# Performance work log

Measured on AMD Instinct MI355X. Metric: run time of the kernel, lower is better.

The kernel has to match this reference:

```python
import jax, jax.numpy as jnp
import numpy as np

N = 50000   # nodes
E = 800000  # edges (avg degree 16)
D = 96      # input feature dim
U = 96      # units (== D, so no dense_i projection)


def _glorot(key, fan_in, fan_out):
    limit = np.sqrt(6.0 / (fan_in + fan_out)).astype(np.float32)
    return jax.random.uniform(key, (fan_in, fan_out), jnp.float32, -limit, limit)


def setup_inputs() -> dict:
    key = jax.random.key(0)
    ks = jax.random.split(key, 8)
    X = jax.random.normal(ks[0], (N, D), jnp.float32)
    row = jax.random.randint(ks[1], (E,), 0, N, jnp.int32)   # destination nodes
    col = jax.random.randint(ks[2], (E,), 0, N, jnp.int32)   # source nodes
    a_vals = jax.random.uniform(ks[3], (E,), jnp.float32)    # adjacency values
    return {
        "X": X,
        "a_vals": a_vals,
        "Wn": _glorot(ks[4], D, U), "bn": jnp.zeros((U,), jnp.float32),
        "Wgi": _glorot(ks[5], D, U), "bgi": jnp.zeros((U,), jnp.float32),
        "Wgn": _glorot(ks[6], U, U), "bgn": jnp.zeros((U,), jnp.float32),
        "row": row, "col": col,
    }


def reference(X, a_vals, Wn, bn, Wgi, bgi, Wgn, bgn, row, col):
    # new_X = dense_n(X); new_X = A @ new_X  (SpMM via gather + segment_sum)
    newX = X @ Wn + bn                       # [N, U]
    msgs = a_vals[:, None] * newX[col]       # [E, U]
    agg = jax.ops.segment_sum(msgs, row, num_segments=N)  # [N, U]
    # gate = sigmoid(dense_gate_i(X) + dense_gate_n(agg))
    gate = jax.nn.sigmoid(X @ Wgi + bgi + agg @ Wgn + bgn)
    # units == inp_dim -> no dense_i; gated residual combine
    return agg * gate + X * (1.0 - gate)
```

## Files before the change

kernel.cpp:

```cpp
#include <hip/hip_runtime.h>
#include <math.h>


#define DU 96
#define DU4 24
#define NSUB 64
#define NGRP 8
#define HMAX 6656

typedef unsigned int uint;
typedef unsigned short ushort;
typedef __attribute__((ext_vector_type(8))) short short8;
typedef __attribute__((ext_vector_type(4))) float f32x4;

__device__ inline uint bf16r(float x) {
  uint u = __float_as_uint(x);
  return (u + 0x7FFFu + ((u >> 16) & 1u)) >> 16;
}

__global__ __launch_bounds__(256) void k_fuse1(
    const float* __restrict__ X, const float* __restrict__ Wn,
    const float* __restrict__ bn, const float* __restrict__ Wgi,
    const float* __restrict__ Wgn, const int* __restrict__ row,
    ushort* __restrict__ Xb, ushort* __restrict__ newXb,
    ushort* __restrict__ WTgi, ushort* __restrict__ WTgn,
    ushort* __restrict__ pc, int N, int E, int ntile) {
  __shared__ __align__(16) char smem[31744];
  ushort* WL = (ushort*)smem;
  typedef ushort XsRow[104];
  XsRow* Xs = (XsRow*)(smem + 18432);
  const int tid = threadIdx.x;
  const int lane = tid & 63, w = tid >> 6;
  const int m = lane & 15, q = lane >> 4;

  if ((int)blockIdx.x < ntile) {
    if (blockIdx.x == 0) {
      for (int i = tid; i < DU * DU; i += 256) {
        int n = i / DU, k = i % DU;
        WTgi[i] = (ushort)bf16r(Wgi[k * DU + n]);
      }
    } else if (blockIdx.x == 1) {
      for (int i = tid; i < DU * DU; i += 256) {
        int n = i / DU, k = i % DU;
        WTgn[i] = (ushort)bf16r(Wgn[k * DU + n]);
      }
    }
    for (int idx = tid; idx < 9216; idx += 256) {
      int j = idx & 7, ln = (idx >> 3) & 63, tk = idx >> 9;
      int ks = tk / 6, t = tk % 6;
      int k = ks * 32 + (ln >> 4) * 8 + j;
      int n = t * 16 + (ln & 15);
      WL[idx] = (ushort)bf16r(Wn[k * DU + n]);
    }
    const int row0 = blockIdx.x * 64;
    for (int i = tid; i < 64 * 48; i += 256) {
      int r = i / 48, cu = i % 48;
      int gr = row0 + r;
      uint packed = 0;
      if (gr < N) {
        float2 v = ((const float2*)X)[(size_t)gr * 48 + cu];
        packed = bf16r(v.x) | (bf16r(v.y) << 16);
        ((uint*)Xb)[(size_t)gr * 48 + cu] = packed;
      }
      *(uint*)&Xs[r][cu * 2] = packed;
    }
    __syncthreads();

    f32x4 acc[6];
#pragma unroll
    for (int t = 0; t < 6; ++t) acc[t] = (f32x4){0.f, 0.f, 0.f, 0.f};
#pragma unroll
    for (int ks = 0; ks < 3; ++ks) {
      short8 af = *(const short8*)&Xs[w * 16 + m][ks * 32 + q * 8];
#pragma unroll
      for (int t = 0; t < 6; ++t) {
        short8 bf = *(const short8*)&WL[((ks * 6 + t) * 64 + lane) * 8];
        acc[t] = __builtin_amdgcn_mfma_f32_16x16x32_bf16(af, bf, acc[t], 0, 0, 0);
      }
    }
    __syncthreads();
#pragma unroll
    for (int t = 0; t < 6; ++t) {
      int c = t * 16 + m;
      float bb = bn[c];
#pragma unroll
      for (int i = 0; i < 4; ++i)
        Xs[w * 16 + q * 4 + i][c] = (ushort)bf16r(acc[t][i] + bb);
    }
    __syncthreads();
    for (int i = tid; i < 64 * 48; i += 256) {
      int r = i / 48, cu = i % 48;
      int gr = row0 + r;
      if (gr < N) ((uint*)newXb)[(size_t)gr * 48 + cu] = *(uint*)&Xs[r][cu * 2];
    }
  } else {
    int* hist = (int*)smem;
    const int hb = (int)blockIdx.x - ntile;
    const int g = (int)(blockIdx.x & 7);
    const int sub = hb >> 3;
    const int d0 = (int)((long long)N * g >> 3);
    const int d1 = (int)((long long)N * (g + 1) >> 3);
    const int hs = d1 - d0;
    for (int j = tid; j < hs; j += 256) hist[j] = 0;
    __syncthreads();
    const int e0 = (int)(((long long)E * sub) >> 6);
    const int e1 = (int)(((long long)E * (sub + 1)) >> 6);
    int i = e0 + tid;
    for (; i + 1792 < e1; i += 2048) {
      int a0 = row[i], a1 = row[i + 256], a2 = row[i + 512], a3 = row[i + 768];
      int a4 = row[i + 1024], a5 = row[i + 1280], a6 = row[i + 1536], a7 = row[i + 1792];
      if (a0 >= d0 && a0 < d1) atomicAdd(&hist[a0 - d0], 1);
      if (a1 >= d0 && a1 < d1) atomicAdd(&hist[a1 - d0], 1);
      if (a2 >= d0 && a2 < d1) atomicAdd(&hist[a2 - d0], 1);
      if (a3 >= d0 && a3 < d1) atomicAdd(&hist[a3 - d0], 1);
      if (a4 >= d0 && a4 < d1) atomicAdd(&hist[a4 - d0], 1);
      if (a5 >= d0 && a5 < d1) atomicAdd(&hist[a5 - d0], 1);
      if (a6 >= d0 && a6 < d1) atomicAdd(&hist[a6 - d0], 1);
      if (a7 >= d0 && a7 < d1) atomicAdd(&hist[a7 - d0], 1);
    }
    for (; i < e1; i += 256) {
      int d = row[i];
      if (d >= d0 && d < d1) atomicAdd(&hist[d - d0], 1);
    }
    __syncthreads();
    for (int j = tid; j < hs; j += 256) pc[(size_t)sub * N + d0 + j] = (ushort)hist[j];
  }
}

__global__ __launch_bounds__(256) void k_colsum(const ushort* __restrict__ pc,
                                                ushort* __restrict__ psub, int N) {
  int d2 = (blockIdx.x * 256 + threadIdx.x) * 2;
  if (d2 >= N) return;
  int runLo = 0, runHi = 0;
#pragma unroll 8
  for (int s = 0; s < NSUB; ++s) {
    uint v = *(const uint*)(pc + (size_t)s * N + d2);
    *(uint*)(psub + (size_t)s * N + d2) = (uint)runLo | ((uint)runHi << 16);
    runLo += (int)(v & 0xFFFFu);
    runHi += (int)(v >> 16);
  }
}

__global__ __launch_bounds__(1024) void k_scan(const ushort* __restrict__ pc,
                                               const ushort* __restrict__ psub,
                                               int* __restrict__ off, int N) {
  __shared__ int ws[16];
  __shared__ int carry_s;
  const ushort* pcL = pc + (size_t)(NSUB - 1) * N;
  const ushort* psL = psub + (size_t)(NSUB - 1) * N;
  const int tid = threadIdx.x;
  const int lane = tid & 63, wid = tid >> 6;
  if (tid == 0) carry_s = 0;
  __syncthreads();
  const int PT = 8;
  const int CH = 1024 * PT;
  for (int base = 0; base < N; base += CH) {
    int idx = base + tid * PT;
    int tot[PT];
    int s = 0;
    if (idx < N) {
      uint4 a = *(const uint4*)(pcL + idx);
      uint4 b = *(const uint4*)(psL + idx);
      tot[0] = (int)(a.x & 0xFFFFu) + (int)(b.x & 0xFFFFu);
      tot[1] = (int)(a.x >> 16) + (int)(b.x >> 16);
      tot[2] = (int)(a.y & 0xFFFFu) + (int)(b.y & 0xFFFFu);
      tot[3] = (int)(a.y >> 16) + (int)(b.y >> 16);
      tot[4] = (int)(a.z & 0xFFFFu) + (int)(b.z & 0xFFFFu);
      tot[5] = (int)(a.z >> 16) + (int)(b.z >> 16);
      tot[6] = (int)(a.w & 0xFFFFu) + (int)(b.w & 0xFFFFu);
      tot[7] = (int)(a.w >> 16) + (int)(b.w >> 16);
#pragma unroll
      for (int j = 0; j < PT; ++j) s += tot[j];
    } else {
#pragma unroll
      for (int j = 0; j < PT; ++j) tot[j] = 0;
    }
    int incl = s;
#pragma unroll
    for (int d = 1; d < 64; d <<= 1) {
      int t = __shfl_up(incl, d, 64);
      if (lane >= d) incl += t;
    }
    if (lane == 63) ws[wid] = incl;
    __syncthreads();
    int carry = carry_s;
    int wexcl = 0;
#pragma unroll
    for (int k = 0; k < 16; ++k)
      if (k < wid) wexcl += ws[k];
    int running = carry + wexcl + (incl - s);
    if (idx < N) {
      int4 o1, o2;
      o1.x = running; running += tot[0];
      o1.y = running; running += tot[1];
      o1.z = running; running += tot[2];
      o1.w = running; running += tot[3];
      o2.x = running; running += tot[4];
      o2.y = running; running += tot[5];
      o2.z = running; running += tot[6];
      o2.w = running; running += tot[7];
      ((int4*)(off + idx))[0] = o1;
      ((int4*)(off + idx))[1] = o2;
    }
    __syncthreads();
    if (tid == 0) {
      int t16 = 0;
#pragma unroll
      for (int k = 0; k < 16; ++k) t16 += ws[k];
      carry_s += t16;
    }
    __syncthreads();
  }
  if (tid == 0) off[N] = carry_s;
}

__global__ __launch_bounds__(256) void k_scatter(const int* __restrict__ row,
                                                 const int* __restrict__ col,
                                                 const float* __restrict__ a_vals,
                                                 const int* __restrict__ off,
                                                 const ushort* __restrict__ psub,
                                                 int2* __restrict__ ec,
                                                 int N, int E) {
  __shared__ int cur[HMAX];
  const int g = (int)(blockIdx.x & 7);
  const int sub = (int)(blockIdx.x >> 3);
  const int d0 = (int)((long long)N * g >> 3);
  const int d1 = (int)((long long)N * (g + 1) >> 3);
  const int hs = d1 - d0;
  for (int j = threadIdx.x; j < hs; j += 256)
    cur[j] = off[d0 + j] + (int)psub[(size_t)sub * N + d0 + j];
  __syncthreads();
  const int e0 = (int)(((long long)E * sub) >> 6);
  const int e1 = (int)(((long long)E * (sub + 1)) >> 6);
  int i = e0 + (int)threadIdx.x;
  for (; i + 1792 < e1; i += 2048) {
    int a0 = row[i], a1 = row[i + 256], a2 = row[i + 512], a3 = row[i + 768];
    int a4 = row[i + 1024], a5 = row[i + 1280], a6 = row[i + 1536], a7 = row[i + 1792];
    if (a0 >= d0 && a0 < d1) {
      int s = atomicAdd(&cur[a0 - d0], 1);
      ec[s] = make_int2(col[i], __float_as_int(a_vals[i]));
    }
    if (a1 >= d0 && a1 < d1) {
      int s = atomicAdd(&cur[a1 - d0], 1);
      ec[s] = make_int2(col[i + 256], __float_as_int(a_vals[i + 256]));
    }
    if (a2 >= d0 && a2 < d1) {
      int s = atomicAdd(&cur[a2 - d0], 1);
      ec[s] = make_int2(col[i + 512], __float_as_int(a_vals[i + 512]));
    }
    if (a3 >= d0 && a3 < d1) {
      int s = atomicAdd(&cur[a3 - d0], 1);
      ec[s] = make_int2(col[i + 768], __float_as_int(a_vals[i + 768]));
    }
    if (a4 >= d0 && a4 < d1) {
      int s = atomicAdd(&cur[a4 - d0], 1);
      ec[s] = make_int2(col[i + 1024], __float_as_int(a_vals[i + 1024]));
    }
    if (a5 >= d0 && a5 < d1) {
      int s = atomicAdd(&cur[a5 - d0], 1);
      ec[s] = make_int2(col[i + 1280], __float_as_int(a_vals[i + 1280]));
    }
    if (a6 >= d0 && a6 < d1) {
      int s = atomicAdd(&cur[a6 - d0], 1);
      ec[s] = make_int2(col[i + 1536], __float_as_int(a_vals[i + 1536]));
    }
    if (a7 >= d0 && a7 < d1) {
      int s = atomicAdd(&cur[a7 - d0], 1);
      ec[s] = make_int2(col[i + 1792], __float_as_int(a_vals[i + 1792]));
    }
  }
  for (; i < e1; i += 256) {
    int d = row[i];
    if (d >= d0 && d < d1) {
      int s = atomicAdd(&cur[d - d0], 1);
      ec[s] = make_int2(col[i], __float_as_int(a_vals[i]));
    }
  }
}

__global__ __launch_bounds__(256) void k_agg(const ushort* __restrict__ newXb,
                                             const int* __restrict__ off,
                                             const int2* __restrict__ ec,
                                             ushort* __restrict__ aggb, int N) {
  const int g = (int)(blockIdx.x & 7);
  const int b2 = (int)(blockIdx.x >> 3);
  const int d0 = (int)((long long)N * g >> 3);
  const int ntask = ((int)((long long)N * (g + 1) >> 3) - d0) * 12;
  int i = b2 * 256 + threadIdx.x;
  if (i >= ntask) return;
  int r = d0 + i / 12;
  int c = i % 12;
  int o0 = off[r];
  int e1 = off[r + 1] - o0;
  const int2* ep = ec + o0;
  float accA[8], accB[8];
#pragma unroll
  for (int k = 0; k < 8; ++k) { accA[k] = 0.f; accB[k] = 0.f; }
  int e = 0;
#define GCN_FMA8(ACC, V, A)                                      \
  ACC[0] = fmaf(A, __uint_as_float(V.x << 16), ACC[0]);          \
  ACC[1] = fmaf(A, __uint_as_float(V.x & 0xFFFF0000u), ACC[1]);  \
  ACC[2] = fmaf(A, __uint_as_float(V.y << 16), ACC[2]);          \
  ACC[3] = fmaf(A, __uint_as_float(V.y & 0xFFFF0000u), ACC[3]);  \
  ACC[4] = fmaf(A, __uint_as_float(V.z << 16), ACC[4]);          \
  ACC[5] = fmaf(A, __uint_as_float(V.z & 0xFFFF0000u), ACC[5]);  \
  ACC[6] = fmaf(A, __uint_as_float(V.w << 16), ACC[6]);          \
  ACC[7] = fmaf(A, __uint_as_float(V.w & 0xFFFF0000u), ACC[7])
  for (; e + 8 <= e1; e += 8) {
    int2 p0 = ep[e + 0];
    int2 p1 = ep[e + 1];
    int2 p2 = ep[e + 2];
    int2 p3 = ep[e + 3];
    int2 p4 = ep[e + 4];
    int2 p5 = ep[e + 5];
    int2 p6 = ep[e + 6];
    int2 p7 = ep[e + 7];
    uint4 v0 = *(const uint4*)(newXb + (size_t)p0.x * DU + c * 8);
    uint4 v1 = *(const uint4*)(newXb + (size_t)p1.x * DU + c * 8);
    uint4 v2 = *(const uint4*)(newXb + (size_t)p2.x * DU + c * 8);
    uint4 v3 = *(const uint4*)(newXb + (size_t)p3.x * DU + c * 8);
    uint4 v4 = *(const uint4*)(newXb + (size_t)p4.x * DU + c * 8);
    uint4 v5 = *(const uint4*)(newXb + (size_t)p5.x * DU + c * 8);
    uint4 v6 = *(const uint4*)(newXb + (size_t)p6.x * DU + c * 8);
    uint4 v7 = *(const uint4*)(newXb + (size_t)p7.x * DU + c * 8);
    float a0 = __int_as_float(p0.y), a1 = __int_as_float(p1.y);
    float a2 = __int_as_float(p2.y), a3 = __int_as_float(p3.y);
    float a4 = __int_as_float(p4.y), a5 = __int_as_float(p5.y);
    float a6 = __int_as_float(p6.y), a7 = __int_as_float(p7.y);
    GCN_FMA8(accA, v0, a0);
    GCN_FMA8(accB, v1, a1);
    GCN_FMA8(accA, v2, a2);
    GCN_FMA8(accB, v3, a3);
    GCN_FMA8(accA, v4, a4);
    GCN_FMA8(accB, v5, a5);
    GCN_FMA8(accA, v6, a6);
    GCN_FMA8(accB, v7, a7);
  }
  for (; e + 4 <= e1; e += 4) {
    int2 p0 = ep[e + 0];
    int2 p1 = ep[e + 1];
    int2 p2 = ep[e + 2];
    int2 p3 = ep[e + 3];
    uint4 v0 = *(const uint4*)(newXb + (size_t)p0.x * DU + c * 8);
    uint4 v1 = *(const uint4*)(newXb + (size_t)p1.x * DU + c * 8);
    uint4 v2 = *(const uint4*)(newXb + (size_t)p2.x * DU + c * 8);
    uint4 v3 = *(const uint4*)(newXb + (size_t)p3.x * DU + c * 8);
    float a0 = __int_as_float(p0.y), a1 = __int_as_float(p1.y);
    float a2 = __int_as_float(p2.y), a3 = __int_as_float(p3.y);
    GCN_FMA8(accA, v0, a0);
    GCN_FMA8(accB, v1, a1);
    GCN_FMA8(accA, v2, a2);
    GCN_FMA8(accB, v3, a3);
  }
  for (; e < e1; ++e) {
    int2 p = ep[e];
    uint4 v = *(const uint4*)(newXb + (size_t)p.x * DU + c * 8);
    float a = __int_as_float(p.y);
    GCN_FMA8(accA, v, a);
  }
#undef GCN_FMA8
#pragma unroll
  for (int k = 0; k < 8; ++k) accA[k] += accB[k];
  uint4 o;
  o.x = bf16r(accA[0]) | (bf16r(accA[1]) << 16);
  o.y = bf16r(accA[2]) | (bf16r(accA[3]) << 16);
  o.z = bf16r(accA[4]) | (bf16r(accA[5]) << 16);
  o.w = bf16r(accA[6]) | (bf16r(accA[7]) << 16);
  *(uint4*)(aggb + (size_t)r * DU + c * 8) = o;
}

__global__ __launch_bounds__(256) void k_gateM(const ushort* __restrict__ Xb,
                                               const ushort* __restrict__ aggb,
                                               const ushort* __restrict__ WTgi,
                                               const ushort* __restrict__ WTgn,
                                               const float* __restrict__ bgi,
                                               const float* __restrict__ bgn,
                                               const float* __restrict__ X,
                                               float* __restrict__ Out, int N) {
  __shared__ float Gs[64][100];
  const int tid = threadIdx.x;
  const int lane = tid & 63, w = tid >> 6;
  const int m = lane & 15, q = lane >> 4;
  const int row0 = blockIdx.x * 64;
  int ar = row0 + w * 16 + m;
  if (ar > N - 1) ar = N - 1;

  f32x4 acc[6];
#pragma unroll
  for (int t = 0; t < 6; ++t) acc[t] = (f32x4){0.f, 0.f, 0.f, 0.f};

#pragma unroll
  for (int ks = 0; ks < 3; ++ks) {
    short8 af = *(const short8*)(Xb + (size_t)ar * DU + ks * 32 + q * 8);
#pragma unroll
    for (int t = 0; t < 6; ++t) {
      short8 bf = *(const short8*)(WTgi + (size_t)(t * 16 + m) * DU + ks * 32 + q * 8);
      acc[t] = __builtin_amdgcn_mfma_f32_16x16x32_bf16(af, bf, acc[t], 0, 0, 0);
    }
  }
#pragma unroll
  for (int ks = 0; ks < 3; ++ks) {
    short8 af = *(const short8*)(aggb + (size_t)ar * DU + ks * 32 + q * 8);
#pragma unroll
    for (int t = 0; t < 6; ++t) {
      short8 bf = *(const short8*)(WTgn + (size_t)(t * 16 + m) * DU + ks * 32 + q * 8);
      acc[t] = __builtin_amdgcn_mfma_f32_16x16x32_bf16(af, bf, acc[t], 0, 0, 0);
    }
  }

#pragma unroll
  for (int t = 0; t < 6; ++t) {
    int c = t * 16 + m;
    float bb = bgi[c] + bgn[c];
#pragma unroll
    for (int i = 0; i < 4; ++i) {
      float z = acc[t][i] + bb;
      Gs[w * 16 + q * 4 + i][c] = 1.f / (1.f + __expf(-z));
    }
  }
  __syncthreads();

  for (int j = tid; j < 64 * DU4; j += 256) {
    int r = j / DU4, c = j % DU4;
    int gr = row0 + r;
    if (gr < N) {
      float4 xv = ((const float4*)X)[(size_t)gr * DU4 + c];
      uint2 av = ((const uint2*)aggb)[(size_t)gr * DU4 + c];
      float a0 = __uint_as_float(av.x << 16);
      float a1 = __uint_as_float(av.x & 0xFFFF0000u);
      float a2 = __uint_as_float(av.y << 16);
      float a3 = __uint_as_float(av.y & 0xFFFF0000u);
      const float* gp = &Gs[r][c * 4];
      float4 o;
      o.x = xv.x + gp[0] * (a0 - xv.x);
      o.y = xv.y + gp[1] * (a1 - xv.y);
      o.z = xv.z + gp[2] * (a2 - xv.z);
      o.w = xv.w + gp[3] * (a3 - xv.w);
      ((float4*)Out)[(size_t)gr * DU4 + c] = o;
    }
  }
}

extern "C" void kernel_launch(void* const* d_in, const int* in_sizes, int n_in,
                              void* d_out, int out_size, void* d_ws, size_t ws_size,
                              hipStream_t stream) {
  const float* X      = (const float*)d_in[0];
  const float* a_vals = (const float*)d_in[1];
  const float* Wn     = (const float*)d_in[2];
  const float* bn     = (const float*)d_in[3];
  const float* Wgi    = (const float*)d_in[4];
  const float* bgi    = (const float*)d_in[5];
  const float* Wgn    = (const float*)d_in[6];
  const float* bgn    = (const float*)d_in[7];
  const int*   row    = (const int*)d_in[8];
  const int*   col    = (const int*)d_in[9];
  float* out = (float*)d_out;

  const int N = in_sizes[0] / DU;
  const int E = in_sizes[1];
  const int ntile = (N + 63) / 64;
  const int G1 = ntile + NSUB * NGRP;

  int2*   ec    = (int2*)d_ws;
  ushort* Xb    = (ushort*)(ec + (size_t)E);
  ushort* newXb = Xb + (size_t)N * DU;
  ushort* aggb  = newXb + (size_t)N * DU;
  ushort* WTgi  = aggb + (size_t)N * DU;
  ushort* WTgn  = WTgi + DU * DU;
  int*    off   = (int*)(WTgn + DU * DU);
  ushort* pc    = (ushort*)(off + ((N + 4) & ~3));
  ushort* psub  = pc + (size_t)NSUB * N;

  const int aggBPG = (int)(((long long)N * 12 / 8 + 255) / 256);

  k_fuse1  <<<G1, 256, 0, stream>>>(X, Wn, bn, Wgi, Wgn, row,
                                    Xb, newXb, WTgi, WTgn, pc, N, E, ntile);
  k_colsum <<<(N / 2 + 255) / 256, 256, 0, stream>>>(pc, psub, N);
  k_scan   <<<1, 1024, 0, stream>>>(pc, psub, off, N);
  k_scatter<<<NSUB * NGRP, 256, 0, stream>>>(row, col, a_vals, off, psub, ec, N, E);
  k_agg    <<<aggBPG * NGRP, 256, 0, stream>>>(newXb, off, ec, aggb, N);
  k_gateM  <<<ntile, 256, 0, stream>>>(Xb, aggb, WTgi, WTgn, bgi, bgn, X, out, N);
}
```

Measured before the change: 196.6 us.

## Fuse aggregation into gate kernel and merge colsum/scan into per-group prep

The SpMM aggregation is fused into the gate kernel, so per-tile aggregates stay in shared memory as fp32 and are never written to or read back from a bf16 buffer. The column-sum and single-block scan are replaced by one kernel with 8 blocks that scans each destination group independently, using fixed padded per-group capacities in the edge buffer so no global scan is needed. NSUB is halved to 32 to shorten the histogram and colsum work. In exchange, the fused kernel runs only ntile blocks, each doing a serial gather before its MFMA work, which lowers parallelism in the gather phase. The padded capacity assumes no group exceeds E/8 plus 16384 edges, which holds for uniform random rows but could overflow on skewed graphs.

```diff
diff --git a/kernel.cpp b/kernel.cpp
--- a/kernel.cpp
+++ b/kernel.cpp
@@ -4,9 +4,10 @@
 
 #define DU 96
 #define DU4 24
-#define NSUB 64
+#define NSUB 32
 #define NGRP 8
 #define HMAX 6656
+#define CAPG_PAD 16384
 
 typedef unsigned int uint;
 typedef unsigned short ushort;
@@ -103,8 +104,8 @@
     const int hs = d1 - d0;
     for (int j = tid; j < hs; j += 256) hist[j] = 0;
     __syncthreads();
-    const int e0 = (int)(((long long)E * sub) >> 6);
-    const int e1 = (int)(((long long)E * (sub + 1)) >> 6);
+    const int e0 = (int)(((long long)E * sub) / NSUB);
+    const int e1 = (int)(((long long)E * (sub + 1)) / NSUB);
     int i = e0 + tid;
     for (; i + 1792 < e1; i += 2048) {
       int a0 = row[i], a1 = row[i + 256], a2 = row[i + 512], a3 = row[i + 768];
@@ -127,91 +128,63 @@
   }
 }
 
-__global__ __launch_bounds__(256) void k_colsum(const ushort* __restrict__ pc,
-                                                ushort* __restrict__ psub, int N) {
-  int d2 = (blockIdx.x * 256 + threadIdx.x) * 2;
-  if (d2 >= N) return;
-  int runLo = 0, runHi = 0;
-#pragma unroll 8
-  for (int s = 0; s < NSUB; ++s) {
-    uint v = *(const uint*)(pc + (size_t)s * N + d2);
-    *(uint*)(psub + (size_t)s * N + d2) = (uint)runLo | ((uint)runHi << 16);
-    runLo += (int)(v & 0xFFFFu);
-    runHi += (int)(v >> 16);
-  }
-}
-
-__global__ __launch_bounds__(1024) void k_scan(const ushort* __restrict__ pc,
-                                               const ushort* __restrict__ psub,
-                                               int* __restrict__ off, int N) {
+__global__ __launch_bounds__(1024) void k_prep(const ushort* __restrict__ pc,
+                                               ushort* __restrict__ psub,
+                                               ushort* __restrict__ deg,
+                                               int* __restrict__ off,
+                                               int N, int E) {
+  __shared__ ushort degs[HMAX];
   __shared__ int ws[16];
-  __shared__ int carry_s;
-  const ushort* pcL = pc + (size_t)(NSUB - 1) * N;
-  const ushort* psL = psub + (size_t)(NSUB - 1) * N;
+  const int g = blockIdx.x;
   const int tid = threadIdx.x;
   const int lane = tid & 63, wid = tid >> 6;
-  if (tid == 0) carry_s = 0;
+  const int d0 = (int)((long long)N * g >> 3);
+  const int d1 = (int)((long long)N * (g + 1) >> 3);
+  const int hs = d1 - d0;
+  for (int j2 = tid * 2; j2 < hs; j2 += 2048) {
+    int d2 = d0 + j2;
+    int runLo = 0, runHi = 0;
+#pragma unroll 8
+    for (int s = 0; s < NSUB; ++s) {
+      uint v = *(const uint*)(pc + (size_t)s * N + d2);
+      *(uint*)(psub + (size_t)s * N + d2) = (uint)runLo | ((uint)runHi << 16);
+      runLo += (int)(v & 0xFFFFu);
+      runHi += (int)(v >> 16);
+    }
+    uint dpair = (uint)runLo | ((uint)runHi << 16);
+    *(uint*)&degs[j2] = dpair;
+    *(uint*)(deg + d2) = dpair;
+  }
   __syncthreads();
   const int PT = 8;
-  const int CH = 1024 * PT;
-  for (int base = 0; base < N; base += CH) {
-    int idx = base + tid * PT;
-    int tot[PT];
-    int s = 0;
-    if (idx < N) {
-      uint4 a = *(const uint4*)(pcL + idx);
-      uint4 b = *(const uint4*)(psL + idx);
-      tot[0] = (int)(a.x & 0xFFFFu) + (int)(b.x & 0xFFFFu);
-      tot[1] = (int)(a.x >> 16) + (int)(b.x >> 16);
-      tot[2] = (int)(a.y & 0xFFFFu) + (int)(b.y & 0xFFFFu);
-      tot[3] = (int)(a.y >> 16) + (int)(b.y >> 16);
-      tot[4] = (int)(a.z & 0xFFFFu) + (int)(b.z & 0xFFFFu);
-      tot[5] = (int)(a.z >> 16) + (int)(b.z >> 16);
-      tot[6] = (int)(a.w & 0xFFFFu) + (int)(b.w & 0xFFFFu);
-      tot[7] = (int)(a.w >> 16) + (int)(b.w >> 16);
-#pragma unroll
-      for (int j = 0; j < PT; ++j) s += tot[j];
-    } else {
-#pragma unroll
-      for (int j = 0; j < PT; ++j) tot[j] = 0;
-    }
-    int incl = s;
-#pragma unroll
-    for (int d = 1; d < 64; d <<= 1) {
-      int t = __shfl_up(incl, d, 64);
-      if (lane >= d) incl += t;
-    }
-    if (lane == 63) ws[wid] = incl;
-    __syncthreads();
-    int carry = carry_s;
-    int wexcl = 0;
-#pragma unroll
-    for (int k = 0; k < 16; ++k)
-      if (k < wid) wexcl += ws[k];
-    int running = carry + wexcl + (incl - s);
-    if (idx < N) {
-      int4 o1, o2;
-      o1.x = running; running += tot[0];
-      o1.y = running; running += tot[1];
-      o1.z = running; running += tot[2];
-      o1.w = running; running += tot[3];
-      o2.x = running; running += tot[4];
-      o2.y = running; running += tot[5];
-      o2.z = running; running += tot[6];
-      o2.w = running; running += tot[7];
-      ((int4*)(off + idx))[0] = o1;
-      ((int4*)(off + idx))[1] = o2;
-    }
-    __syncthreads();
-    if (tid == 0) {
-      int t16 = 0;
-#pragma unroll
-      for (int k = 0; k < 16; ++k) t16 += ws[k];
-      carry_s += t16;
-    }
-    __syncthreads();
-  }
-  if (tid == 0) off[N] = carry_s;
+  const int j0 = tid * PT;
+  int v[PT];
+  int s = 0;
+#pragma unroll
+  for (int k = 0; k < PT; ++k) {
+    int j = j0 + k;
+    v[k] = (j < hs) ? (int)degs[j] : 0;
+    s += v[k];
+  }
+  int incl = s;
+#pragma unroll
+  for (int dlt = 1; dlt < 64; dlt <<= 1) {
+    int t = __shfl_up(incl, dlt, 64);
+    if (lane >= dlt) incl += t;
+  }
+  if (lane == 63) ws[wid] = incl;
+  __syncthreads();
+  int wexcl = 0;
+#pragma unroll
+  for (int k = 0; k < 16; ++k)
+    if (k < wid) wexcl += ws[k];
+  const int capg = (E >> 3) + CAPG_PAD;
+  int running = g * capg + wexcl + (incl - s);
+#pragma unroll
+  for (int k = 0; k < PT; ++k) {
+    int j = j0 + k;
+    if (j < hs) { off[d0 + j] = running; running += v[k]; }
+  }
 }
 
 __global__ __launch_bounds__(256) void k_scatter(const int* __restrict__ row,
@@ -230,8 +203,8 @@
   for (int j = threadIdx.x; j < hs; j += 256)
     cur[j] = off[d0 + j] + (int)psub[(size_t)sub * N + d0 + j];
   __syncthreads();
-  const int e0 = (int)(((long long)E * sub) >> 6);
-  const int e1 = (int)(((long long)E * (sub + 1)) >> 6);
+  const int e0 = (int)(((long long)E * sub) / NSUB);
+  const int e1 = (int)(((long long)E * (sub + 1)) / NSUB);
   int i = e0 + (int)threadIdx.x;
   for (; i + 1792 < e1; i += 2048) {
     int a0 = row[i], a1 = row[i + 256], a2 = row[i + 512], a3 = row[i + 768];
@@ -278,25 +251,20 @@
   }
 }
 
-__global__ __launch_bounds__(256) void k_agg(const ushort* __restrict__ newXb,
-                                             const int* __restrict__ off,
-                                             const int2* __restrict__ ec,
-                                             ushort* __restrict__ aggb, int N) {
-  const int g = (int)(blockIdx.x & 7);
-  const int b2 = (int)(blockIdx.x >> 3);
-  const int d0 = (int)((long long)N * g >> 3);
-  const int ntask = ((int)((long long)N * (g + 1) >> 3) - d0) * 12;
-  int i = b2 * 256 + threadIdx.x;
-  if (i >= ntask) return;
-  int r = d0 + i / 12;
-  int c = i % 12;
-  int o0 = off[r];
-  int e1 = off[r + 1] - o0;
-  const int2* ep = ec + o0;
-  float accA[8], accB[8];
-#pragma unroll
-  for (int k = 0; k < 8; ++k) { accA[k] = 0.f; accB[k] = 0.f; }
-  int e = 0;
+__global__ __launch_bounds__(256) void k_aggGate(
+    const ushort* __restrict__ Xb, const ushort* __restrict__ newXb,
+    const int* __restrict__ off, const ushort* __restrict__ deg,
+    const int2* __restrict__ ec, const ushort* __restrict__ WTgi,
+    const ushort* __restrict__ WTgn, const float* __restrict__ bgi,
+    const float* __restrict__ bgn, const float* __restrict__ X,
+    float* __restrict__ Out, int N) {
+  __shared__ float As[64][104];
+  __shared__ float Gs[64][100];
+  const int tid = threadIdx.x;
+  const int lane = tid & 63, w = tid >> 6;
+  const int m = lane & 15, q = lane >> 4;
+  const int row0 = blockIdx.x * 64;
+
 #define GCN_FMA8(ACC, V, A)                                      \
   ACC[0] = fmaf(A, __uint_as_float(V.x << 16), ACC[0]);          \
   ACC[1] = fmaf(A, __uint_as_float(V.x & 0xFFFF0000u), ACC[1]);  \
@@ -306,89 +274,82 @@
   ACC[5] = fmaf(A, __uint_as_float(V.z & 0xFFFF0000u), ACC[5]);  \
   ACC[6] = fmaf(A, __uint_as_float(V.w << 16), ACC[6]);          \
   ACC[7] = fmaf(A, __uint_as_float(V.w & 0xFFFF0000u), ACC[7])
-  for (; e + 8 <= e1; e += 8) {
-    int2 p0 = ep[e + 0];
-    int2 p1 = ep[e + 1];
-    int2 p2 = ep[e + 2];
-    int2 p3 = ep[e + 3];
-    int2 p4 = ep[e + 4];
-    int2 p5 = ep[e + 5];
-    int2 p6 = ep[e + 6];
-    int2 p7 = ep[e + 7];
-    uint4 v0 = *(const uint4*)(newXb + (size_t)p0.x * DU + c * 8);
-    uint4 v1 = *(const uint4*)(newXb + (size_t)p1.x * DU + c * 8);
-    uint4 v2 = *(const uint4*)(newXb + (size_t)p2.x * DU + c * 8);
-    uint4 v3 = *(const uint4*)(newXb + (size_t)p3.x * DU + c * 8);
-    uint4 v4 = *(const uint4*)(newXb + (size_t)p4.x * DU + c * 8);
-    uint4 v5 = *(const uint4*)(newXb + (size_t)p5.x * DU + c * 8);
-    uint4 v6 = *(const uint4*)(newXb + (size_t)p6.x * DU + c * 8);
-    uint4 v7 = *(const uint4*)(newXb + (size_t)p7.x * DU + c * 8);
-    float a0 = __int_as_float(p0.y), a1 = __int_as_float(p1.y);
-    float a2 = __int_as_float(p2.y), a3 = __int_as_float(p3.y);
-    float a4 = __int_as_float(p4.y), a5 = __int_as_float(p5.y);
-    float a6 = __int_as_float(p6.y), a7 = __int_as_float(p7.y);
-    GCN_FMA8(accA, v0, a0);
-    GCN_FMA8(accB, v1, a1);
-    GCN_FMA8(accA, v2, a2);
-    GCN_FMA8(accB, v3, a3);
-    GCN_FMA8(accA, v4, a4);
-    GCN_FMA8(accB, v5, a5);
-    GCN_FMA8(accA, v6, a6);
-    GCN_FMA8(accB, v7, a7);
-  }
-  for (; e + 4 <= e1; e += 4) {
-    int2 p0 = ep[e + 0];
-    int2 p1 = ep[e + 1];
-    int2 p2 = ep[e + 2];
-    int2 p3 = ep[e + 3];
-    uint4 v0 = *(const uint4*)(newXb + (size_t)p0.x * DU + c * 8);
-    uint4 v1 = *(const uint4*)(newXb + (size_t)p1.x * DU + c * 8);
-    uint4 v2 = *(const uint4*)(newXb + (size_t)p2.x * DU + c * 8);
-    uint4 v3 = *(const uint4*)(newXb + (size_t)p3.x * DU + c * 8);
-    float a0 = __int_as_float(p0.y), a1 = __int_as_float(p1.y);
-    float a2 = __int_as_float(p2.y), a3 = __int_as_float(p3.y);
-    GCN_FMA8(accA, v0, a0);
-    GCN_FMA8(accB, v1, a1);
-    GCN_FMA8(accA, v2, a2);
-    GCN_FMA8(accB, v3, a3);
-  }
-  for (; e < e1; ++e) {
-    int2 p = ep[e];
-    uint4 v = *(const uint4*)(newXb + (size_t)p.x * DU + c * 8);
-    float a = __int_as_float(p.y);
-    GCN_FMA8(accA, v, a);
+  for (int t = tid; t < 64 * 12; t += 256) {
+    const int rl = t / 12, c = t % 12;
+    const int r = row0 + rl;
+    float accA[8], accB[8];
+#pragma unroll
+    for (int k = 0; k < 8; ++k) { accA[k] = 0.f; accB[k] = 0.f; }
+    if (r < N) {
+      const int2* ep = ec + off[r];
+      const int e1 = (int)deg[r];
+      int e = 0;
+      for (; e + 8 <= e1; e += 8) {
+        int2 p0 = ep[e + 0];
+        int2 p1 = ep[e + 1];
+        int2 p2 = ep[e + 2];
+        int2 p3 = ep[e + 3];
+        int2 p4 = ep[e + 4];
+        int2 p5 = ep[e + 5];
+        int2 p6 = ep[e + 6];
+        int2 p7 = ep[e + 7];
+        uint4 v0 = *(const uint4*)(newXb + (size_t)p0.x * DU + c * 8);
+        uint4 v1 = *(const uint4*)(newXb + (size_t)p1.x * DU + c * 8);
+        uint4 v2 = *(const uint4*)(newXb + (size_t)p2.x * DU + c * 8);
+        uint4 v3 = *(const uint4*)(newXb + (size_t)p3.x * DU + c * 8);
+        uint4 v4 = *(const uint4*)(newXb + (size_t)p4.x * DU + c * 8);
+        uint4 v5 = *(const uint4*)(newXb + (size_t)p5.x * DU + c * 8);
+        uint4 v6 = *(const uint4*)(newXb + (size_t)p6.x * DU + c * 8);
+        uint4 v7 = *(const uint4*)(newXb + (size_t)p7.x * DU + c * 8);
+        float a0 = __int_as_float(p0.y), a1 = __int_as_float(p1.y);
+        float a2 = __int_as_float(p2.y), a3 = __int_as_float(p3.y);
+        float a4 = __int_as_float(p4.y), a5 = __int_as_float(p5.y);
+        float a6 = __int_as_float(p6.y), a7 = __int_as_float(p7.y);
+        GCN_FMA8(accA, v0, a0);
+        GCN_FMA8(accB, v1, a1);
+        GCN_FMA8(accA, v2, a2);
+        GCN_FMA8(accB, v3, a3);
+        GCN_FMA8(accA, v4, a4);
+        GCN_FMA8(accB, v5, a5);
+        GCN_FMA8(accA, v6, a6);
+        GCN_FMA8(accB, v7, a7);
+      }
+      for (; e + 4 <= e1; e += 4) {
+        int2 p0 = ep[e + 0];
+        int2 p1 = ep[e + 1];
+        int2 p2 = ep[e + 2];
+        int2 p3 = ep[e + 3];
+        uint4 v0 = *(const uint4*)(newXb + (size_t)p0.x * DU + c * 8);
+        uint4 v1 = *(const uint4*)(newXb + (size_t)p1.x * DU + c * 8);
+        uint4 v2 = *(const uint4*)(newXb + (size_t)p2.x * DU + c * 8);
+        uint4 v3 = *(const uint4*)(newXb + (size_t)p3.x * DU + c * 8);
+        float a0 = __int_as_float(p0.y), a1 = __int_as_float(p1.y);
+        float a2 = __int_as_float(p2.y), a3 = __int_as_float(p3.y);
+        GCN_FMA8(accA, v0, a0);
+        GCN_FMA8(accB, v1, a1);
+        GCN_FMA8(accA, v2, a2);
+        GCN_FMA8(accB, v3, a3);
+      }
+      for (; e < e1; ++e) {
+        int2 p = ep[e];
+        uint4 v = *(const uint4*)(newXb + (size_t)p.x * DU + c * 8);
+        float a = __int_as_float(p.y);
+        GCN_FMA8(accA, v, a);
+      }
+    }
+#pragma unroll
+    for (int k = 0; k < 8; ++k) accA[k] += accB[k];
+    *(float4*)&As[rl][c * 8 + 0] = make_float4(accA[0], accA[1], accA[2], accA[3]);
+    *(float4*)&As[rl][c * 8 + 4] = make_float4(accA[4], accA[5], accA[6], accA[7]);
   }
 #undef GCN_FMA8
-#pragma unroll
-  for (int k = 0; k < 8; ++k) accA[k] += accB[k];
-  uint4 o;
-  o.x = bf16r(accA[0]) | (bf16r(accA[1]) << 16);
-  o.y = bf16r(accA[2]) | (bf16r(accA[3]) << 16);
-  o.z = bf16r(accA[4]) | (bf16r(accA[5]) << 16);
-  o.w = bf16r(accA[6]) | (bf16r(accA[7]) << 16);
-  *(uint4*)(aggb + (size_t)r * DU + c * 8) = o;
-}
-
-__global__ __launch_bounds__(256) void k_gateM(const ushort* __restrict__ Xb,
-                                               const ushort* __restrict__ aggb,
-                                               const ushort* __restrict__ WTgi,
-                                               const ushort* __restrict__ WTgn,
-                                               const float* __restrict__ bgi,
-                                               const float* __restrict__ bgn,
-                                               const float* __restrict__ X,
-                                               float* __restrict__ Out, int N) {
-  __shared__ float Gs[64][100];
-  const int tid = threadIdx.x;
-  const int lane = tid & 63, w = tid >> 6;
-  const int m = lane & 15, q = lane >> 4;
-  const int row0 = blockIdx.x * 64;
+  __syncthreads();
+
   int ar = row0 + w * 16 + m;
   if (ar > N - 1) ar = N - 1;
-
   f32x4 acc[6];
 #pragma unroll
   for (int t = 0; t < 6; ++t) acc[t] = (f32x4){0.f, 0.f, 0.f, 0.f};
-
 #pragma unroll
   for (int ks = 0; ks < 3; ++ks) {
     short8 af = *(const short8*)(Xb + (size_t)ar * DU + ks * 32 + q * 8);
@@ -398,16 +359,22 @@
       acc[t] = __builtin_amdgcn_mfma_f32_16x16x32_bf16(af, bf, acc[t], 0, 0, 0);
     }
   }
+  const int rl = w * 16 + m;
 #pragma unroll
   for (int ks = 0; ks < 3; ++ks) {
-    short8 af = *(const short8*)(aggb + (size_t)ar * DU + ks * 32 + q * 8);
+    float4 u0 = *(const float4*)&As[rl][ks * 32 + q * 8];
+    float4 u1 = *(const float4*)&As[rl][ks * 32 + q * 8 + 4];
+    short8 af;
+    af[0] = (short)bf16r(u0.x); af[1] = (short)bf16r(u0.y);
+    af[2] = (short)bf16r(u0.z); af[3] = (short)bf16r(u0.w);
+    af[4] = (short)bf16r(u1.x); af[5] = (short)bf16r(u1.y);
+    af[6] = (short)bf16r(u1.z); af[7] = (short)bf16r(u1.w);
 #pragma unroll
     for (int t = 0; t < 6; ++t) {
       short8 bf = *(const short8*)(WTgn + (size_t)(t * 16 + m) * DU + ks * 32 + q * 8);
       acc[t] = __builtin_amdgcn_mfma_f32_16x16x32_bf16(af, bf, acc[t], 0, 0, 0);
     }
   }
-
 #pragma unroll
   for (int t = 0; t < 6; ++t) {
     int c = t * 16 + m;
@@ -425,17 +392,13 @@
     int gr = row0 + r;
     if (gr < N) {
       float4 xv = ((const float4*)X)[(size_t)gr * DU4 + c];
-      uint2 av = ((const uint2*)aggb)[(size_t)gr * DU4 + c];
-      float a0 = __uint_as_float(av.x << 16);
-      float a1 = __uint_as_float(av.x & 0xFFFF0000u);
-      float a2 = __uint_as_float(av.y << 16);
-      float a3 = __uint_as_float(av.y & 0xFFFF0000u);
+      float4 av = *(const float4*)&As[r][c * 4];
       const float* gp = &Gs[r][c * 4];
       float4 o;
-      o.x = xv.x + gp[0] * (a0 - xv.x);
-      o.y = xv.y + gp[1] * (a1 - xv.y);
-      o.z = xv.z + gp[2] * (a2 - xv.z);
-      o.w = xv.w + gp[3] * (a3 - xv.w);
+      o.x = xv.x + gp[0] * (av.x - xv.x);
+      o.y = xv.y + gp[1] * (av.y - xv.y);
+      o.z = xv.z + gp[2] * (av.z - xv.z);
+      o.w = xv.w + gp[3] * (av.w - xv.w);
       ((float4*)Out)[(size_t)gr * DU4 + c] = o;
     }
   }
@@ -460,24 +423,22 @@
   const int E = in_sizes[1];
   const int ntile = (N + 63) / 64;
   const int G1 = ntile + NSUB * NGRP;
+  const int capg = (E >> 3) + CAPG_PAD;
 
   int2*   ec    = (int2*)d_ws;
-  ushort* Xb    = (ushort*)(ec + (size_t)E);
+  ushort* Xb    = (ushort*)(ec + (size_t)NGRP * capg);
   ushort* newXb = Xb + (size_t)N * DU;
-  ushort* aggb  = newXb + (size_t)N * DU;
-  ushort* WTgi  = aggb + (size_t)N * DU;
+  ushort* WTgi  = newXb + (size_t)N * DU;
   ushort* WTgn  = WTgi + DU * DU;
   int*    off   = (int*)(WTgn + DU * DU);
-  ushort* pc    = (ushort*)(off + ((N + 4) & ~3));
+  ushort* deg   = (ushort*)(off + ((N + 3) & ~3));
+  ushort* pc    = deg + (((size_t)N + 7) & ~7ull);
   ushort* psub  = pc + (size_t)NSUB * N;
-
-  const int aggBPG = (int)(((long long)N * 12 / 8 + 255) / 256);
 
   k_fuse1  <<<G1, 256, 0, stream>>>(X, Wn, bn, Wgi, Wgn, row,
                                     Xb, newXb, WTgi, WTgn, pc, N, E, ntile);
-  k_colsum <<<(N / 2 + 255) / 256, 256, 0, stream>>>(pc, psub, N);
-  k_scan   <<<1, 1024, 0, stream>>>(pc, psub, off, N);
+  k_prep   <<<NGRP, 1024, 0, stream>>>(pc, psub, deg, off, N, E);
   k_scatter<<<NSUB * NGRP, 256, 0, stream>>>(row, col, a_vals, off, psub, ec, N, E);
-  k_agg    <<<aggBPG * NGRP, 256, 0, stream>>>(newXb, off, ec, aggb, N);
-  k_gateM  <<<ntile, 256, 0, stream>>>(Xb, aggb, WTgi, WTgn, bgi, bgn, X, out, N);
-}
+  k_aggGate<<<ntile, 256, 0, stream>>>(Xb, newXb, off, deg, ec, WTgi, WTgn,
+                                       bgi, bgn, X, out, N);
+}
```

Measured after the change: 218.9 us. +11.3%, slower.
